# Kernel tuning notes

Measured on AMD Instinct MI355X. Metric: run time of the kernel, lower is better.

## Reference

```python
import jax, jax.numpy as jnp
import numpy as np

_POWERS = jnp.array([128, 64, 32, 16, 8, 4, 2, 1], dtype=jnp.int32)


def _unpack_ternary(pos_mask, neg_mask, in_dim):
    """Unpack uint8-style bitmasks [out, in//8] to ternary {-1,0,+1} [out, in]."""
    out_dim = pos_mask.shape[0]
    pos_bits = ((pos_mask[:, :, None] & _POWERS) != 0).astype(jnp.int8)  # [out, in/8, 8]
    neg_bits = ((neg_mask[:, :, None] & _POWERS) != 0).astype(jnp.int8)
    w_t = (pos_bits - neg_bits).reshape(out_dim, -1)[:, :in_dim]
    return w_t


def setup_inputs() -> dict:
    key = jax.random.key(0)
    k1, k2, k3, k4, k5 = jax.random.split(key, 5)
    TOKENS, IN, OUT = 4096, 4096, 4096
    x = jax.random.normal(k1, (TOKENS, IN), dtype=jnp.float32)
    pos_mask = jax.random.randint(k2, (OUT, IN // 8), 0, 256, dtype=jnp.int32)
    neg_mask = jax.random.randint(k3, (OUT, IN // 8), 0, 256, dtype=jnp.int32)
    scale = jax.random.uniform(k4, (), dtype=jnp.float32) * 0.05 + 0.01  # absmean scale
    bias = jax.random.normal(k5, (OUT,), dtype=jnp.float32)
    return {"x": x, "pos_mask": pos_mask, "neg_mask": neg_mask, "scale": scale,
            "bias": bias, "in_features": IN}


def reference(x, pos_mask, neg_mask, scale, bias, in_features):
    # y = scale * (x @ W_pos.T - x @ W_neg.T) + bias == scale * (x @ w_t.T) + bias,
    # since pos - neg == w_t exactly (entries in {-1,0,+1}).
    w_t = _unpack_ternary(pos_mask, neg_mask, in_features).astype(x.dtype)  # [out, in]
    y = scale * jnp.einsum('ti,oi->to', x, w_t) + bias
    return y
```

## Files before the change

kernel.cpp:

```cpp
#include <hip/hip_runtime.h>
#include <hip/hip_bf16.h>

typedef unsigned short ushort_t;
typedef unsigned int uint_t;

typedef __attribute__((ext_vector_type(8))) short bf16x8;
typedef __attribute__((ext_vector_type(4))) float f32x4;
typedef __attribute__((ext_vector_type(8))) unsigned short u16x8;

constexpr int Mdim = 4096;
constexpr int Ndim = 4096;
constexpr int Kdim = 4096;
constexpr int K2 = Kdim * 2;
constexpr int NIT = Kdim / 128;

__device__ __forceinline__ ushort_t f2bf(float f) {
  uint_t u = __float_as_uint(f);
  u += 0x7fffu + ((u >> 16) & 1u);
  return (ushort_t)(u >> 16);
}

__global__ void __launch_bounds__(256) cvt_x_kernel(const float* __restrict__ x,
                                                    ushort_t* __restrict__ xb) {
  const size_t t = (size_t)blockIdx.x * 256 + threadIdx.x;
  const float4* p = reinterpret_cast<const float4*>(x) + t * 2;
  float4 a = p[0], b = p[1];
  u16x8 o;
  o[0] = f2bf(a.x); o[1] = f2bf(a.y); o[2] = f2bf(a.z); o[3] = f2bf(a.w);
  o[4] = f2bf(b.x); o[5] = f2bf(b.y); o[6] = f2bf(b.z); o[7] = f2bf(b.w);
  *reinterpret_cast<u16x8*>(xb + t * 8) = o;
}

__global__ void __launch_bounds__(256) unpack_w_kernel(const int* __restrict__ pos,
                                                       const int* __restrict__ neg,
                                                       ushort_t* __restrict__ wb) {
  const size_t t = (size_t)blockIdx.x * 256 + threadIdx.x;
  const int4 p = reinterpret_cast<const int4*>(pos)[t];
  const int4 q = reinterpret_cast<const int4*>(neg)[t];
  const int pv[4] = {p.x, p.y, p.z, p.w};
  const int nv[4] = {q.x, q.y, q.z, q.w};
  ushort_t* dst = wb + t * 32;
#pragma unroll
  for (int e = 0; e < 4; ++e) {
    u16x8 v;
#pragma unroll
    for (int j = 0; j < 8; ++j) {
      const int pb = (pv[e] >> (7 - j)) & 1;
      const int nb = (nv[e] >> (7 - j)) & 1;
      const int d = pb - nb;
      v[j] = (d == 1) ? (ushort_t)0x3F80 : ((d == -1) ? (ushort_t)0xBF80 : (ushort_t)0);
    }
    *reinterpret_cast<u16x8*>(dst + e * 8) = v;
  }
}

#define GLD16(gp, lp)                                                     \
  __builtin_amdgcn_global_load_lds(                                       \
      (const __attribute__((address_space(1))) void*)(gp),                \
      (__attribute__((address_space(3))) void*)(lp), 16, 0, 0)

#define VMCNT(N) asm volatile("s_waitcnt vmcnt(" #N ")" ::: "memory")

#define BARRIER() do {                          \
  __builtin_amdgcn_sched_barrier(0);            \
  __builtin_amdgcn_s_barrier();                 \
  __builtin_amdgcn_sched_barrier(0);            \
} while (0)


#define STAGE_A(BUF, HALF, KT) do {                                                    \
  const char* g_ = Ab + gAoff + (size_t)(HALF) * (128 * (size_t)K2) + (size_t)(KT) * 128; \
  char* l_ = ldsw + (BUF) * 32768 + (HALF) * 16384;                                    \
  GLD16(g_, l_);                                                                       \
  GLD16(g_ + (size_t)64 * K2, l_ + 8192);                                              \
} while (0)

#define STAGE_B(BUF, HALF, KT) do {                                                    \
  const char* g_ = Bb + gBoff + (size_t)(HALF) * (128 * (size_t)K2) + (size_t)(KT) * 128; \
  char* l_ = ldsw + 65536 + (BUF) * 32768 + (HALF) * 16384;                            \
  GLD16(g_, l_);                                                                       \
  GLD16(g_ + (size_t)64 * K2, l_ + 8192);                                              \
} while (0)

#define LDA(BUF, M, KK) (*(const bf16x8*)(lds + (BUF) * 32768 + aRowBase + (M) * 2048 + acol[KK]))
#define LDB(BUF, N, KK) (*(const bf16x8*)(lds + 65536 + (BUF) * 32768 + bRowBase + (N) * 2048 + acol[KK]))

#define READS_A(BANK, RB, RQ) do {                                                     \
  af##BANK[0] = LDA(RB, 2*(RQ),   0); af##BANK[1] = LDA(RB, 2*(RQ),   1);              \
  af##BANK[2] = LDA(RB, 2*(RQ)+1, 0); af##BANK[3] = LDA(RB, 2*(RQ)+1, 1);              \
} while (0)

#define READS_B(CB) do {                                                               \
  _Pragma("unroll")                                                                    \
  for (int n_ = 0; n_ < 4; ++n_) { vb[n_][0] = LDB(CB, n_, 0); vb[n_][1] = LDB(CB, n_, 1); } \
} while (0)

#define MFMA16(BANK, Q) do {                                                           \
  __builtin_amdgcn_s_setprio(1);                                                       \
  _Pragma("unroll")                                                                    \
  for (int n_ = 0; n_ < 4; ++n_) {                                                     \
    acc[2*(Q)][n_]   = __builtin_amdgcn_mfma_f32_16x16x32_bf16(af##BANK[0], vb[n_][0], acc[2*(Q)][n_],   0, 0, 0); \
    acc[2*(Q)+1][n_] = __builtin_amdgcn_mfma_f32_16x16x32_bf16(af##BANK[2], vb[n_][0], acc[2*(Q)+1][n_], 0, 0, 0); \
  }                                                                                    \
  _Pragma("unroll")                                                                    \
  for (int n_ = 0; n_ < 4; ++n_) {                                                     \
    acc[2*(Q)][n_]   = __builtin_amdgcn_mfma_f32_16x16x32_bf16(af##BANK[1], vb[n_][1], acc[2*(Q)][n_],   0, 0, 0); \
    acc[2*(Q)+1][n_] = __builtin_amdgcn_mfma_f32_16x16x32_bf16(af##BANK[3], vb[n_][1], acc[2*(Q)+1][n_], 0, 0, 0); \
  }                                                                                    \
  __builtin_amdgcn_s_setprio(0);                                                       \
} while (0)

__global__ void __launch_bounds__(512, 2) gemm_kernel(const ushort_t* __restrict__ A,
                                                      const ushort_t* __restrict__ B,
                                                      float* __restrict__ C,
                                                      const float* __restrict__ scale_p,
                                                      const float* __restrict__ bias) {
  __shared__ char lds[131072];

  const int bid = blockIdx.x;
  const int swz = (bid & 7) * 32 + (bid >> 3);
  const int m0 = (swz >> 4) * 256;
  const int n0 = (swz & 15) * 256;

  const int tid = threadIdx.x;
  const int wid = tid >> 6;
  const int lane = tid & 63;
  const int wr = wid >> 2;
  const int wc = wid & 3;

  float sv = *scale_p;
  float bv[4];
#pragma unroll
  for (int n = 0; n < 4; ++n) bv[n] = bias[n0 + wc * 64 + n * 16 + (lane & 15)];
  asm volatile("" : "+v"(sv), "+v"(bv[0]), "+v"(bv[1]), "+v"(bv[2]), "+v"(bv[3]));

  const int srow = tid >> 3;
  const int scol = 16 * ((tid & 7) ^ (srow & 7));
  const char* Ab = (const char*)A;
  const char* Bb = (const char*)B;
  const size_t gAoff = (size_t)(m0 + srow) * K2 + scol;
  const size_t gBoff = (size_t)(n0 + srow) * K2 + scol;
  char* ldsw = lds + wid * 1024;

  const int acol[2] = { (0  + ((lane >> 4) << 4)) ^ ((lane & 7) << 4),
                        (64 + ((lane >> 4) << 4)) ^ ((lane & 7) << 4) };
  const int aRowBase = wr * 16384 + (lane & 15) * 128;
  const int bRowBase = (wc >> 1) * 16384 + ((wc & 1) * 64 + (lane & 15)) * 128;

  f32x4 acc[8][4] = {};
  bf16x8 af0[4], af1[4];
  bf16x8 vb[4][2];

  STAGE_B(0, 0, 0); STAGE_B(0, 1, 0);
  STAGE_A(0, 0, 0); STAGE_A(0, 1, 0);
  STAGE_B(1, 0, 1); STAGE_B(1, 1, 1);
  VMCNT(4);
  BARRIER();
  READS_A(0, 0, 0);

#pragma unroll 1
  for (int i = 0; i < NIT - 1; ++i) {
    const int t1 = 2 * i + 1, tn = 2 * i + 2;
    BARRIER(); STAGE_A(1, 0, t1); STAGE_A(1, 1, t1);
               READS_B(0); READS_A(1, 0, 1); MFMA16(0, 0);
    BARRIER(); STAGE_B(0, 0, tn);
               READS_A(0, 0, 2); MFMA16(1, 1);
    BARRIER(); STAGE_B(0, 1, tn);
               READS_A(1, 0, 3); MFMA16(0, 2);
    VMCNT(4);
    BARRIER(); READS_A(0, 1, 0); MFMA16(1, 3);
    BARRIER(); STAGE_A(0, 0, tn);
               READS_B(1); READS_A(1, 1, 1); MFMA16(0, 0);
    BARRIER(); STAGE_A(0, 1, tn);
               READS_A(0, 1, 2); MFMA16(1, 1);
    BARRIER(); STAGE_B(1, 0, t1 + 2);
               READS_A(1, 1, 3); MFMA16(0, 2);
    VMCNT(2);
    BARRIER(); STAGE_B(1, 1, t1 + 2);
               READS_A(0, 0, 0); MFMA16(1, 3);
  }
  {
    BARRIER(); STAGE_A(1, 0, 2 * NIT - 1); STAGE_A(1, 1, 2 * NIT - 1);
               READS_B(0); READS_A(1, 0, 1); MFMA16(0, 0);
    BARRIER(); READS_A(0, 0, 2); MFMA16(1, 1);
    BARRIER(); READS_A(1, 0, 3); MFMA16(0, 2);
    VMCNT(0);
    BARRIER(); READS_A(0, 1, 0); MFMA16(1, 3);
    BARRIER(); READS_B(1); READS_A(1, 1, 1); MFMA16(0, 0);
    BARRIER(); READS_A(0, 1, 2); MFMA16(1, 1);
    BARRIER(); READS_A(1, 1, 3); MFMA16(0, 2);
    BARRIER(); MFMA16(1, 3);
  }

  const int row0 = m0 + wr * 128 + ((lane >> 4) << 2);
  const int col0 = n0 + wc * 64 + (lane & 15);
#pragma unroll
  for (int m = 0; m < 8; ++m)
#pragma unroll
    for (int n = 0; n < 4; ++n) {
      const int c = col0 + n * 16;
#pragma unroll
      for (int k = 0; k < 4; ++k)
        C[(size_t)(row0 + m * 16 + k) * Ndim + c] = sv * acc[m][n][k] + bv[n];
    }
}

extern "C" void kernel_launch(void* const* d_in, const int* in_sizes, int n_in,
                              void* d_out, int out_size, void* d_ws, size_t ws_size,
                              hipStream_t stream) {
  const float* x = (const float*)d_in[0];
  const int* pos = (const int*)d_in[1];
  const int* neg = (const int*)d_in[2];
  const float* scale = (const float*)d_in[3];
  const float* bias = (const float*)d_in[4];
  float* out = (float*)d_out;

  ushort_t* xb = (ushort_t*)d_ws;
  ushort_t* wb = xb + (size_t)Mdim * Kdim;

  cvt_x_kernel<<<(Mdim * Kdim) / (256 * 8), 256, 0, stream>>>(x, xb);
  unpack_w_kernel<<<(Ndim * (Kdim / 8)) / (256 * 4), 256, 0, stream>>>(pos, neg, wb);
  gemm_kernel<<<dim3((Mdim / 256) * (Ndim / 256)), 512, 0, stream>>>(xb, wb, out, scale, bias);
}
```

Baseline: 239.9 us.

## Merge prep kernels into one launch and split B fragment reads across MFMA halves

Combines the x-to-bf16 conversion and the ternary weight unpack into a single launch whose blocks branch on block index, removing one kernel launch and the gap between the two. In the GEMM main loop, B fragments are now loaded in two k-halves, and the next tile's first half is prefetched in the middle of the preceding MFMA group. The aim is to hide LDS read latency behind matrix ops and shorten the stall at the start of each phase. It keeps the same register footprint but changes where the LDS reads fall relative to the barriers.

```diff
diff --git a/kernel.cpp b/kernel.cpp
--- a/kernel.cpp
+++ b/kernel.cpp
@@ -20,37 +20,42 @@
   return (ushort_t)(u >> 16);
 }
 
-__global__ void __launch_bounds__(256) cvt_x_kernel(const float* __restrict__ x,
-                                                    ushort_t* __restrict__ xb) {
-  const size_t t = (size_t)blockIdx.x * 256 + threadIdx.x;
-  const float4* p = reinterpret_cast<const float4*>(x) + t * 2;
-  float4 a = p[0], b = p[1];
-  u16x8 o;
-  o[0] = f2bf(a.x); o[1] = f2bf(a.y); o[2] = f2bf(a.z); o[3] = f2bf(a.w);
-  o[4] = f2bf(b.x); o[5] = f2bf(b.y); o[6] = f2bf(b.z); o[7] = f2bf(b.w);
-  *reinterpret_cast<u16x8*>(xb + t * 8) = o;
-}
-
-__global__ void __launch_bounds__(256) unpack_w_kernel(const int* __restrict__ pos,
-                                                       const int* __restrict__ neg,
-                                                       ushort_t* __restrict__ wb) {
-  const size_t t = (size_t)blockIdx.x * 256 + threadIdx.x;
-  const int4 p = reinterpret_cast<const int4*>(pos)[t];
-  const int4 q = reinterpret_cast<const int4*>(neg)[t];
-  const int pv[4] = {p.x, p.y, p.z, p.w};
-  const int nv[4] = {q.x, q.y, q.z, q.w};
-  ushort_t* dst = wb + t * 32;
-#pragma unroll
-  for (int e = 0; e < 4; ++e) {
-    u16x8 v;
-#pragma unroll
-    for (int j = 0; j < 8; ++j) {
-      const int pb = (pv[e] >> (7 - j)) & 1;
-      const int nb = (nv[e] >> (7 - j)) & 1;
-      const int d = pb - nb;
-      v[j] = (d == 1) ? (ushort_t)0x3F80 : ((d == -1) ? (ushort_t)0xBF80 : (ushort_t)0);
+constexpr int CVT_BLOCKS = (Mdim * Kdim) / (256 * 8);
+constexpr int UNPACK_BLOCKS = (Ndim * (Kdim / 8)) / (256 * 4);
+
+__global__ void __launch_bounds__(256) prep_kernel(const float* __restrict__ x,
+                                                   ushort_t* __restrict__ xb,
+                                                   const int* __restrict__ pos,
+                                                   const int* __restrict__ neg,
+                                                   ushort_t* __restrict__ wb) {
+  const int b = blockIdx.x;
+  if (b < CVT_BLOCKS) {
+    const size_t t = (size_t)b * 256 + threadIdx.x;
+    const float4* p = reinterpret_cast<const float4*>(x) + t * 2;
+    float4 a = p[0], c = p[1];
+    u16x8 o;
+    o[0] = f2bf(a.x); o[1] = f2bf(a.y); o[2] = f2bf(a.z); o[3] = f2bf(a.w);
+    o[4] = f2bf(c.x); o[5] = f2bf(c.y); o[6] = f2bf(c.z); o[7] = f2bf(c.w);
+    *reinterpret_cast<u16x8*>(xb + t * 8) = o;
+  } else {
+    const size_t t = (size_t)(b - CVT_BLOCKS) * 256 + threadIdx.x;
+    const int4 p = reinterpret_cast<const int4*>(pos)[t];
+    const int4 q = reinterpret_cast<const int4*>(neg)[t];
+    const int pv[4] = {p.x, p.y, p.z, p.w};
+    const int nv[4] = {q.x, q.y, q.z, q.w};
+    ushort_t* dst = wb + t * 32;
+#pragma unroll
+    for (int e = 0; e < 4; ++e) {
+      u16x8 v;
+#pragma unroll
+      for (int j = 0; j < 8; ++j) {
+        const int pb = (pv[e] >> (7 - j)) & 1;
+        const int nb = (nv[e] >> (7 - j)) & 1;
+        const int d = pb - nb;
+        v[j] = (d == 1) ? (ushort_t)0x3F80 : ((d == -1) ? (ushort_t)0xBF80 : (ushort_t)0);
+      }
+      *reinterpret_cast<u16x8*>(dst + e * 8) = v;
     }
-    *reinterpret_cast<u16x8*>(dst + e * 8) = v;
   }
 }
 
@@ -90,22 +95,17 @@
   af##BANK[2] = LDA(RB, 2*(RQ)+1, 0); af##BANK[3] = LDA(RB, 2*(RQ)+1, 1);              \
 } while (0)
 
-#define READS_B(CB) do {                                                               \
-  _Pragma("unroll")                                                                    \
-  for (int n_ = 0; n_ < 4; ++n_) { vb[n_][0] = LDB(CB, n_, 0); vb[n_][1] = LDB(CB, n_, 1); } \
-} while (0)
-
-#define MFMA16(BANK, Q) do {                                                           \
+#define READS_B_HALF(CB, KK) do {                                                      \
+  vb[0][KK] = LDB(CB, 0, KK); vb[1][KK] = LDB(CB, 1, KK);                              \
+  vb[2][KK] = LDB(CB, 2, KK); vb[3][KK] = LDB(CB, 3, KK);                              \
+} while (0)
+
+#define MFMA8(BANK, Q, KK) do {                                                        \
   __builtin_amdgcn_s_setprio(1);                                                       \
   _Pragma("unroll")                                                                    \
   for (int n_ = 0; n_ < 4; ++n_) {                                                     \
-    acc[2*(Q)][n_]   = __builtin_amdgcn_mfma_f32_16x16x32_bf16(af##BANK[0], vb[n_][0], acc[2*(Q)][n_],   0, 0, 0); \
-    acc[2*(Q)+1][n_] = __builtin_amdgcn_mfma_f32_16x16x32_bf16(af##BANK[2], vb[n_][0], acc[2*(Q)+1][n_], 0, 0, 0); \
-  }                                                                                    \
-  _Pragma("unroll")                                                                    \
-  for (int n_ = 0; n_ < 4; ++n_) {                                                     \
-    acc[2*(Q)][n_]   = __builtin_amdgcn_mfma_f32_16x16x32_bf16(af##BANK[1], vb[n_][1], acc[2*(Q)][n_],   0, 0, 0); \
-    acc[2*(Q)+1][n_] = __builtin_amdgcn_mfma_f32_16x16x32_bf16(af##BANK[3], vb[n_][1], acc[2*(Q)+1][n_], 0, 0, 0); \
+    acc[2*(Q)][n_]   = __builtin_amdgcn_mfma_f32_16x16x32_bf16(af##BANK[0+(KK)], vb[n_][KK], acc[2*(Q)][n_],   0, 0, 0); \
+    acc[2*(Q)+1][n_] = __builtin_amdgcn_mfma_f32_16x16x32_bf16(af##BANK[2+(KK)], vb[n_][KK], acc[2*(Q)+1][n_], 0, 0, 0); \
   }                                                                                    \
   __builtin_amdgcn_s_setprio(0);                                                       \
 } while (0)
@@ -157,39 +157,47 @@
   VMCNT(4);
   BARRIER();
   READS_A(0, 0, 0);
+  READS_B_HALF(0, 0);
 
 #pragma unroll 1
   for (int i = 0; i < NIT - 1; ++i) {
     const int t1 = 2 * i + 1, tn = 2 * i + 2;
     BARRIER(); STAGE_A(1, 0, t1); STAGE_A(1, 1, t1);
-               READS_B(0); READS_A(1, 0, 1); MFMA16(0, 0);
+               READS_B_HALF(0, 1); READS_A(1, 0, 1);
+               MFMA8(0, 0, 0); MFMA8(0, 0, 1);
     BARRIER(); STAGE_B(0, 0, tn);
-               READS_A(0, 0, 2); MFMA16(1, 1);
+               READS_A(0, 0, 2); MFMA8(1, 1, 0); MFMA8(1, 1, 1);
     BARRIER(); STAGE_B(0, 1, tn);
-               READS_A(1, 0, 3); MFMA16(0, 2);
+               READS_A(1, 0, 3); MFMA8(0, 2, 0); MFMA8(0, 2, 1);
     VMCNT(4);
-    BARRIER(); READS_A(0, 1, 0); MFMA16(1, 3);
+    BARRIER(); READS_A(0, 1, 0);
+               MFMA8(1, 3, 0); READS_B_HALF(1, 0); MFMA8(1, 3, 1);
     BARRIER(); STAGE_A(0, 0, tn);
-               READS_B(1); READS_A(1, 1, 1); MFMA16(0, 0);
+               READS_B_HALF(1, 1); READS_A(1, 1, 1);
+               MFMA8(0, 0, 0); MFMA8(0, 0, 1);
     BARRIER(); STAGE_A(0, 1, tn);
-               READS_A(0, 1, 2); MFMA16(1, 1);
+               READS_A(0, 1, 2); MFMA8(1, 1, 0); MFMA8(1, 1, 1);
     BARRIER(); STAGE_B(1, 0, t1 + 2);
-               READS_A(1, 1, 3); MFMA16(0, 2);
+               READS_A(1, 1, 3); MFMA8(0, 2, 0); MFMA8(0, 2, 1);
     VMCNT(2);
     BARRIER(); STAGE_B(1, 1, t1 + 2);
-               READS_A(0, 0, 0); MFMA16(1, 3);
+               READS_A(0, 0, 0);
+               MFMA8(1, 3, 0); READS_B_HALF(0, 0); MFMA8(1, 3, 1);
   }
   {
     BARRIER(); STAGE_A(1, 0, 2 * NIT - 1); STAGE_A(1, 1, 2 * NIT - 1);
-               READS_B(0); READS_A(1, 0, 1); MFMA16(0, 0);
-    BARRIER(); READS_A(0, 0, 2); MFMA16(1, 1);
-    BARRIER(); READS_A(1, 0, 3); MFMA16(0, 2);
+               READS_B_HALF(0, 1); READS_A(1, 0, 1);
+               MFMA8(0, 0, 0); MFMA8(0, 0, 1);
+    BARRIER(); READS_A(0, 0, 2); MFMA8(1, 1, 0); MFMA8(1, 1, 1);
+    BARRIER(); READS_A(1, 0, 3); MFMA8(0, 2, 0); MFMA8(0, 2, 1);
     VMCNT(0);
-    BARRIER(); READS_A(0, 1, 0); MFMA16(1, 3);
-    BARRIER(); READS_B(1); READS_A(1, 1, 1); MFMA16(0, 0);
-    BARRIER(); READS_A(0, 1, 2); MFMA16(1, 1);
-    BARRIER(); READS_A(1, 1, 3); MFMA16(0, 2);
-    BARRIER(); MFMA16(1, 3);
+    BARRIER(); READS_A(0, 1, 0);
+               MFMA8(1, 3, 0); READS_B_HALF(1, 0); MFMA8(1, 3, 1);
+    BARRIER(); READS_B_HALF(1, 1); READS_A(1, 1, 1);
+               MFMA8(0, 0, 0); MFMA8(0, 0, 1);
+    BARRIER(); READS_A(0, 1, 2); MFMA8(1, 1, 0); MFMA8(1, 1, 1);
+    BARRIER(); READS_A(1, 1, 3); MFMA8(0, 2, 0); MFMA8(0, 2, 1);
+    BARRIER(); MFMA8(1, 3, 0); MFMA8(1, 3, 1);
   }
 
   const int row0 = m0 + wr * 128 + ((lane >> 4) << 2);
@@ -218,7 +226,6 @@
   ushort_t* xb = (ushort_t*)d_ws;
   ushort_t* wb = xb + (size_t)Mdim * Kdim;
 
-  cvt_x_kernel<<<(Mdim * Kdim) / (256 * 8), 256, 0, stream>>>(x, xb);
-  unpack_w_kernel<<<(Ndim * (Kdim / 8)) / (256 * 4), 256, 0, stream>>>(pos, neg, wb);
+  prep_kernel<<<CVT_BLOCKS + UNPACK_BLOCKS, 256, 0, stream>>>(x, xb, pos, neg, wb);
   gemm_kernel<<<dim3((Mdim / 256) * (Ndim / 256)), 512, 0, stream>>>(xb, wb, out, scale, bias);
 }
```

New measurement: 236.1 us. About the same (-1.6%).
